# Performance work log

Hardware: AMD Instinct MI355X
Metric: run time of the kernel (lower is better)

## Reference

```python
import jax, jax.numpy as jnp
import numpy as np

N, D, T = 8192, 512, 12
EPS = 1e-6


def _ln(x, g, b):
    m = jnp.mean(x, axis=-1, keepdims=True)
    v = jnp.mean((x - m) ** 2, axis=-1, keepdims=True)
    return (x - m) / jnp.sqrt(v + EPS) * g + b


def _cross(x1, x2, Wa, ba, Wb, bb, d1, d2):
    # attn_weights2: [N, N], softmax over dim=1 (rows)
    aw2 = jax.nn.softmax((x1 @ Wa.T + ba) @ x2.T, axis=1)
    fused_x2 = (aw2 @ x2) / jnp.sqrt(jnp.float32(d2))
    aw1 = jax.nn.softmax((x2 @ Wb.T + bb) @ x1.T, axis=1)
    fused_x1 = (aw1 @ x1) / jnp.sqrt(jnp.float32(d1))
    return fused_x1, fused_x2


def setup_inputs() -> dict:
    key = jax.random.key(0)
    ks = jax.random.split(key, 16)
    s = 1.0 / np.sqrt(D)
    inp = {
        'xp': jax.random.normal(ks[0], (N, D), jnp.float32),
        'xm': jax.random.normal(ks[1], (N, D), jnp.float32),
        'xs': jax.random.normal(ks[2], (N, D), jnp.float32),
        'ln_g': jnp.ones((D,), jnp.float32),
        'ln_b': jnp.zeros((D,), jnp.float32),
        # mol cross-attention: linear1 (D->D), linear2 (D->D)
        'W1': jax.random.uniform(ks[3], (D, D), jnp.float32, -s, s),
        'b1': jnp.zeros((D,), jnp.float32),
        'W2': jax.random.uniform(ks[4], (D, D), jnp.float32, -s, s),
        'b2': jnp.zeros((D,), jnp.float32),
        # smile cross-attention
        'W3': jax.random.uniform(ks[5], (D, D), jnp.float32, -s, s),
        'b3': jnp.zeros((D,), jnp.float32),
        'W4': jax.random.uniform(ks[6], (D, D), jnp.float32, -s, s),
        'b4': jnp.zeros((D,), jnp.float32),
        # pred head: 2D -> T
        'Wp': jax.random.uniform(ks[7], (T, 2 * D), jnp.float32, -1.0 / np.sqrt(2 * D), 1.0 / np.sqrt(2 * D)),
        'bp': jnp.zeros((T,), jnp.float32),
        # gate
        't': jnp.full((1,), 0.5, jnp.float32),
        'Wt1': jax.random.uniform(ks[8], (50, 1), jnp.float32, -1.0, 1.0),
        'bt1': jnp.zeros((50,), jnp.float32),
        'Wt2': jax.random.uniform(ks[9], (1, 50), jnp.float32, -1.0 / np.sqrt(50), 1.0 / np.sqrt(50)),
        'bt2': jnp.zeros((1,), jnp.float32),
    }
    return inp


def reference(xp, xm, xs, ln_g, ln_b, W1, b1, W2, b2, W3, b3, W4, b4, Wp, bp, t, Wt1, bt1, Wt2, bt2):
    x1 = _ln(xp, ln_g, ln_b)
    x2 = _ln(xm, ln_g, ln_b)
    x3 = x1  # protein encoded twice with same LayerNorm
    x4 = _ln(xs, ln_g, ln_b)

    f1, f2 = _cross(x1, x2, W1, b1, W2, b2, D, D)
    h12 = jnp.concatenate([f1 + x1, f2 + x2], axis=1)          # [N, 2D]
    out12 = jax.nn.relu(h12) @ Wp.T + bp                        # [N, T]

    f3, f4 = _cross(x3, x4, W3, b3, W4, b4, D, D)
    h34 = jnp.concatenate([f3 + x3, f4 + x4], axis=1)
    out34 = jax.nn.relu(h34) @ Wp.T + bp

    t1 = t @ Wt1.T + bt1                                        # [50]
    t2 = jax.nn.sigmoid(t1 @ Wt2.T + bt2)                       # [1]
    return t2 * out12 + (1.0 - t2) * out34
```

## Files before the change

### kernel.cpp

```cpp
#include <hip/hip_runtime.h>
#include <stdint.h>


#define DEV __device__ __forceinline__
typedef unsigned short u16;
typedef __bf16 bf16x8 __attribute__((ext_vector_type(8)));
typedef float f32x4 __attribute__((ext_vector_type(4)));

constexpr int NR = 8192;
constexpr int DDIM = 512;
constexpr int TOUT = 12;

DEV u16 f2b(float f) {
  uint32_t u = __builtin_bit_cast(uint32_t, f);
  u += 0x7fffu + ((u >> 16) & 1u);
  return (u16)(u >> 16);
}
DEV float b2f(u16 h) {
  uint32_t u = ((uint32_t)h) << 16;
  return __builtin_bit_cast(float, u);
}

__global__ __launch_bounds__(64) void ln_kernel(
    const float* __restrict__ xp, const float* __restrict__ xm,
    const float* __restrict__ xs, const float* __restrict__ g,
    const float* __restrict__ b, u16* __restrict__ o1, u16* __restrict__ o2,
    u16* __restrict__ o4) {
  int row = blockIdx.x;
  int which = blockIdx.y;
  const float* x = which == 0 ? xp : (which == 1 ? xm : xs);
  u16* o = which == 0 ? o1 : (which == 1 ? o2 : o4);
  int lane = threadIdx.x;
  const float4* xr = (const float4*)(x + (size_t)row * DDIM);
  float4 v0 = xr[lane * 2], v1 = xr[lane * 2 + 1];
  float vals[8] = {v0.x, v0.y, v0.z, v0.w, v1.x, v1.y, v1.z, v1.w};
  float s = 0.f, s2 = 0.f;
  for (int j = 0; j < 8; j++) { s += vals[j]; s2 += vals[j] * vals[j]; }
  for (int off = 1; off < 64; off <<= 1) {
    s += __shfl_xor(s, off);
    s2 += __shfl_xor(s2, off);
  }
  float m = s * (1.0f / DDIM);
  float var = s2 * (1.0f / DDIM) - m * m;
  var = fmaxf(var, 0.f);
  float rs = rsqrtf(var + 1e-6f);
  int d0 = lane * 8;
  u16 us[8];
  for (int j = 0; j < 8; j++)
    us[j] = f2b((vals[j] - m) * rs * g[d0 + j] + b[d0 + j]);
  uint4 pk;
  pk.x = (uint32_t)us[0] | ((uint32_t)us[1] << 16);
  pk.y = (uint32_t)us[2] | ((uint32_t)us[3] << 16);
  pk.z = (uint32_t)us[4] | ((uint32_t)us[5] << 16);
  pk.w = (uint32_t)us[6] | ((uint32_t)us[7] << 16);
  *(uint4*)(o + (size_t)row * DDIM + d0) = pk;
}

__global__ __launch_bounds__(256) void wconv_kernel(
    const float* __restrict__ W1, const float* __restrict__ W2,
    const float* __restrict__ W3, const float* __restrict__ W4,
    u16* __restrict__ Wb) {
  int wi = blockIdx.y;
  const float* W = wi == 0 ? W1 : (wi == 1 ? W2 : (wi == 2 ? W3 : W4));
  size_t base = ((size_t)blockIdx.x * 256 + threadIdx.x) * 8;
  const float4* src = (const float4*)(W + base);
  float4 a = src[0], c = src[1];
  float vals[8] = {a.x, a.y, a.z, a.w, c.x, c.y, c.z, c.w};
  u16 us[8];
  for (int j = 0; j < 8; j++) us[j] = f2b(vals[j]);
  uint4 pk;
  pk.x = (uint32_t)us[0] | ((uint32_t)us[1] << 16);
  pk.y = (uint32_t)us[2] | ((uint32_t)us[3] << 16);
  pk.z = (uint32_t)us[4] | ((uint32_t)us[5] << 16);
  pk.w = (uint32_t)us[6] | ((uint32_t)us[7] << 16);
  *(uint4*)(Wb + (size_t)wi * DDIM * DDIM + base) = pk;
}

__global__ __launch_bounds__(256) void transpose_kernel(
    const u16* __restrict__ s1, const u16* __restrict__ s2,
    const u16* __restrict__ s4, u16* __restrict__ t1, u16* __restrict__ t2,
    u16* __restrict__ t4) {
  constexpr int LD = 66;
  __shared__ u16 tile[64 * LD];
  int which = blockIdx.z;
  const u16* src = which == 0 ? s1 : (which == 1 ? s2 : s4);
  u16* dst = which == 0 ? t1 : (which == 1 ? t2 : t4);
  int c0 = blockIdx.x * 64;
  int r0 = blockIdx.y * 64;
  int tid = threadIdx.x;
  for (int c = tid; c < 512; c += 256) {
    int i = c >> 3, j8 = (c & 7) * 8;
    uint4 v = *(const uint4*)(src + (size_t)(r0 + i) * DDIM + c0 + j8);
    uint32_t* dw = (uint32_t*)&tile[i * LD + j8];
    dw[0] = v.x; dw[1] = v.y; dw[2] = v.z; dw[3] = v.w;
  }
  __syncthreads();
  for (int c = tid; c < 512; c += 256) {
    int o = c >> 3, e8 = (c & 7) * 8;
    u16 us[8];
    for (int k = 0; k < 8; k++) us[k] = tile[(e8 + k) * LD + o];
    uint4 pk;
    pk.x = (uint32_t)us[0] | ((uint32_t)us[1] << 16);
    pk.y = (uint32_t)us[2] | ((uint32_t)us[3] << 16);
    pk.z = (uint32_t)us[4] | ((uint32_t)us[5] << 16);
    pk.w = (uint32_t)us[6] | ((uint32_t)us[7] << 16);
    *(uint4*)(dst + (size_t)(c0 + o) * NR + r0 + e8) = pk;
  }
}

template <int MODE>
DEV void gemm_core(const u16* __restrict__ A, const u16* __restrict__ B,
                   u16* __restrict__ C, const float* __restrict__ bias,
                   u16* lds, int K, int lda, int ldb, int ldc, int bx,
                   int by) {
  constexpr int TM = 4, TN = 4;
  u16* Asm = lds;
  u16* Bsm = lds + 4096;
  int tid = threadIdx.x;
  int w = tid >> 6, lane = tid & 63;
  int q = lane >> 4, c16 = lane & 15;
  int n0 = bx * 128, m0 = by * 128;
  int wrow = (w >> 1) * 64, wcol = (w & 1) * 64;
  f32x4 acc[TM][TN] = {};
  for (int k0 = 0; k0 < K; k0 += 32) {
    __syncthreads();
    for (int call = w; call < 16; call += 4) {
      bool isA = call < 8;
      int ci = isA ? call : call - 8;
      int chunk = ci * 64 + lane;
      int row = chunk >> 2;
      int gch = ((chunk & 3) - (row >> 1)) & 3;
      const u16* gp = isA ? (A + (size_t)(m0 + row) * lda + k0 + gch * 8)
                          : (B + (size_t)(n0 + row) * ldb + k0 + gch * 8);
      u16* lp = (isA ? Asm : Bsm) + ci * 512;
      __builtin_amdgcn_global_load_lds(
          (const __attribute__((address_space(1))) void*)gp,
          (__attribute__((address_space(3))) void*)lp, 16, 0, 0);
    }
    __syncthreads();
    bf16x8 af[TM], bfr[TN];
    for (int i = 0; i < TM; i++) {
      int r = wrow + i * 16 + c16;
      af[i] = *(const bf16x8*)&Asm[r * 32 + (((q + (r >> 1)) & 3) * 8)];
    }
    for (int n = 0; n < TN; n++) {
      int r = wcol + n * 16 + c16;
      bfr[n] = *(const bf16x8*)&Bsm[r * 32 + (((q + (r >> 1)) & 3) * 8)];
    }
    for (int i = 0; i < TM; i++)
      for (int n = 0; n < TN; n++)
        acc[i][n] = __builtin_amdgcn_mfma_f32_16x16x32_bf16(af[i], bfr[n],
                                                            acc[i][n], 0, 0, 0);
  }
  for (int h = 0; h < 2; h++) {
    __syncthreads();
    if ((w & 1) == h) {
      for (int i = 0; i < TM; i++) {
        for (int n = 0; n < TN; n++) {
          float bv = 0.f;
          if constexpr (MODE == 0) bv = bias[n0 + wcol + n * 16 + c16];
          for (int r = 0; r < 4; r++) {
            int rl = wrow + i * 16 + q * 4 + r;
            int cl = (n * 16 + c16) ^ ((rl & 7) << 3);
            float v = acc[i][n][r];
            if constexpr (MODE == 0) v += bv;
            if constexpr (MODE == 1) v = __expf(v - 48.0f);
            lds[rl * 64 + cl] = f2b(v);
          }
        }
      }
    }
    __syncthreads();
    for (int rep = 0; rep < 4; rep++) {
      int idx = rep * 256 + tid;
      int row = idx >> 3, seg = idx & 7;
      uint4 vv = ((const uint4*)lds)[row * 8 + (seg ^ (row & 7))];
      *(uint4*)(C + (size_t)(m0 + row) * ldc + n0 + h * 64 + seg * 8) = vv;
    }
  }
}

DEV void pv_body(const u16* __restrict__ A, const u16* __restrict__ B,
                 u16* lds, u16* __restrict__ C, int bx, int by) {
  constexpr int BM = 64, BN = 128, BK = 64;
  int tid = threadIdx.x, w = tid >> 6, lane = tid & 63;
  int q = lane >> 4, c16 = lane & 15;
  int n0 = bx * BN, m0 = by * BM;
  int wr = (w >> 1) * 32, wc = (w & 1) * 64;
  f32x4 acc[2][4] = {};
  f32x4 accl[2] = {};
  bf16x8 ones;
  for (int j = 0; j < 8; j++) ones[j] = (__bf16)1.0f;

  auto stage = [&](int k0, int buf) {
    for (int it = 0; it < 6; it++) {
      int cb = it * 256 + w * 64;
      int c = cb + lane;
      bool isA = cb < 512;
      int ci = isA ? c : c - 512;
      int row = ci >> 3;
      int koff = ((ci & 7) ^ (row & 7)) * 8;
      const u16* gp = isA ? (A + (size_t)(m0 + row) * NR + k0 + koff)
                          : (B + (size_t)(n0 + row) * NR + k0 + koff);
      u16* lp = isA ? (lds + buf * 4096 + cb * 8)
                    : (lds + 8192 + buf * 8192 + (cb - 512) * 8);
      __builtin_amdgcn_global_load_lds(
          (const __attribute__((address_space(1))) void*)gp,
          (__attribute__((address_space(3))) void*)lp, 16, 0, 0);
    }
  };

  stage(0, 0);
  __syncthreads();
  constexpr int KSTEPS = NR / BK;
  for (int ks = 0; ks < KSTEPS; ks++) {
    int cur = ks & 1;
    if (ks + 1 < KSTEPS) stage((ks + 1) * BK, cur ^ 1);
    const u16* Asm = lds + cur * 4096;
    const u16* Bsm = lds + 8192 + cur * 8192;
    for (int kh = 0; kh < 2; kh++) {
      bf16x8 af[2], bfr[4];
      int cl = kh * 4 + q;
      for (int i = 0; i < 2; i++) {
        int r = wr + i * 16 + c16;
        af[i] = *(const bf16x8*)&Asm[r * BK + ((cl ^ (r & 7)) * 8)];
      }
      for (int n = 0; n < 4; n++) {
        int r = wc + n * 16 + c16;
        bfr[n] = *(const bf16x8*)&Bsm[r * BK + ((cl ^ (r & 7)) * 8)];
      }
      for (int i = 0; i < 2; i++)
        accl[i] = __builtin_amdgcn_mfma_f32_16x16x32_bf16(af[i], ones, accl[i],
                                                          0, 0, 0);
      for (int i = 0; i < 2; i++)
        for (int n = 0; n < 4; n++)
          acc[i][n] = __builtin_amdgcn_mfma_f32_16x16x32_bf16(
              af[i], bfr[n], acc[i][n], 0, 0, 0);
    }
    __syncthreads();
  }
  for (int i = 0; i < 2; i++) {
    float invl[4];
    for (int r = 0; r < 4; r++)
      invl[r] = 0.044194173824159216f / accl[i][r];
    for (int n = 0; n < 4; n++) {
      int col = n0 + wc + n * 16 + c16;
      for (int r = 0; r < 4; r++) {
        int row = m0 + wr + i * 16 + q * 4 + r;
        C[(size_t)row * DDIM + col] = f2b(acc[i][n][r] * invl[r]);
      }
    }
  }
}

__global__ __launch_bounds__(256, 4) void scores_kernel(
    const u16* __restrict__ Q, const u16* __restrict__ Kv,
    u16* __restrict__ P) {
  __shared__ u16 lds[8192];
  gemm_core<1>(Q, Kv, P, nullptr, lds, DDIM, DDIM, DDIM, NR, blockIdx.x,
               blockIdx.y);
}

__global__ __launch_bounds__(256, 4) void qproj_kernel(
    const u16* __restrict__ s0, const u16* __restrict__ s1,
    const u16* __restrict__ s2, const u16* __restrict__ s3,
    const u16* __restrict__ Wb, const float* __restrict__ b0,
    const float* __restrict__ b1, const float* __restrict__ b2,
    const float* __restrict__ b3, u16* __restrict__ Qs) {
  __shared__ u16 lds[8192];
  int z = blockIdx.z;
  const u16* A = z == 0 ? s0 : (z == 1 ? s1 : (z == 2 ? s2 : s3));
  const float* bias = z == 0 ? b0 : (z == 1 ? b1 : (z == 2 ? b2 : b3));
  gemm_core<0>(A, Wb + (size_t)z * DDIM * DDIM, Qs + (size_t)z * NR * DDIM,
               bias, lds, DDIM, DDIM, DDIM, DDIM, blockIdx.x, blockIdx.y);
}

__global__ __launch_bounds__(256, 3) void pv_kernel(
    const u16* __restrict__ A, const u16* __restrict__ B,
    u16* __restrict__ C) {
  __shared__ u16 lds[24576];
  pv_body(A, B, lds, C, blockIdx.x, blockIdx.y);
}

__global__ __launch_bounds__(256, 3) void combo_kernel(
    const u16* __restrict__ Pin, const u16* __restrict__ Vt,
    u16* __restrict__ F, const u16* __restrict__ Q,
    const u16* __restrict__ Kv, u16* __restrict__ Pout) {
  __shared__ u16 lds[24576];
  if (blockIdx.x < 512) {
    pv_body(Pin, Vt, lds, F, blockIdx.x & 3, blockIdx.x >> 2);
  } else {
    int b = blockIdx.x - 512;
    gemm_core<1>(Q, Kv, Pout, nullptr, lds, DDIM, DDIM, DDIM, NR, b & 63,
                 b >> 6);
  }
}

__global__ __launch_bounds__(256) void head_kernel(
    const u16* __restrict__ F1, const u16* __restrict__ F2,
    const u16* __restrict__ F3, const u16* __restrict__ F4,
    const u16* __restrict__ x1, const u16* __restrict__ x2,
    const u16* __restrict__ x4, const float* __restrict__ Wp,
    const float* __restrict__ bp, const float* __restrict__ tg,
    const float* __restrict__ Wt1, const float* __restrict__ bt1,
    const float* __restrict__ Wt2, const float* __restrict__ bt2,
    float* __restrict__ out) {
  __shared__ float wps[TOUT * 2 * DDIM];
  __shared__ float t2s;
  int tid = threadIdx.x;
  for (int i = tid; i < TOUT * 2 * DDIM; i += 256) wps[i] = Wp[i];
  if (tid == 0) {
    float s = bt2[0];
    for (int k = 0; k < 50; k++) s += Wt2[k] * (tg[0] * Wt1[k] + bt1[k]);
    t2s = 1.0f / (1.0f + __expf(-s));
  }
  __syncthreads();
  int g = tid >> 5, j = tid & 31;
  size_t m = (size_t)blockIdx.x * 8 + g;
  float a12[TOUT] = {}, a34[TOUT] = {};
  for (int d = j; d < 2 * DDIM; d += 32) {
    float h12, h34;
    if (d < DDIM) {
      float xv = b2f(x1[m * DDIM + d]);
      h12 = b2f(F1[m * DDIM + d]) + xv;
      h34 = b2f(F3[m * DDIM + d]) + xv;
    } else {
      int dd = d - DDIM;
      h12 = b2f(F2[m * DDIM + dd]) + b2f(x2[m * DDIM + dd]);
      h34 = b2f(F4[m * DDIM + dd]) + b2f(x4[m * DDIM + dd]);
    }
    h12 = fmaxf(h12, 0.f);
    h34 = fmaxf(h34, 0.f);
    for (int t = 0; t < TOUT; t++) {
      float wv = wps[t * 2 * DDIM + d];
      a12[t] += h12 * wv;
      a34[t] += h34 * wv;
    }
  }
  for (int off = 1; off < 32; off <<= 1)
    for (int t = 0; t < TOUT; t++) {
      a12[t] += __shfl_xor(a12[t], off);
      a34[t] += __shfl_xor(a34[t], off);
    }
  if (j < TOUT) {
    float t2 = t2s;
    out[m * TOUT + j] = t2 * a12[j] + (1.f - t2) * a34[j] + bp[j];
  }
}

extern "C" void kernel_launch(void* const* d_in, const int* in_sizes, int n_in,
                              void* d_out, int out_size, void* d_ws,
                              size_t ws_size, hipStream_t stream) {
  (void)in_sizes; (void)n_in; (void)out_size;
  const float* xp = (const float*)d_in[0];
  const float* xm = (const float*)d_in[1];
  const float* xs = (const float*)d_in[2];
  const float* ln_g = (const float*)d_in[3];
  const float* ln_b = (const float*)d_in[4];
  const float* Wmat[4] = {(const float*)d_in[5], (const float*)d_in[7],
                          (const float*)d_in[9], (const float*)d_in[11]};
  const float* bvec[4] = {(const float*)d_in[6], (const float*)d_in[8],
                          (const float*)d_in[10], (const float*)d_in[12]};
  const float* Wp = (const float*)d_in[13];
  const float* bp = (const float*)d_in[14];
  const float* tg = (const float*)d_in[15];
  const float* Wt1 = (const float*)d_in[16];
  const float* bt1 = (const float*)d_in[17];
  const float* Wt2 = (const float*)d_in[18];
  const float* bt2 = (const float*)d_in[19];
  float* out = (float*)d_out;

  char* ws = (char*)d_ws;
  const size_t MB = 1ull << 20;
  u16* x1b = (u16*)(ws + 0 * MB);
  u16* x2b = (u16*)(ws + 8 * MB);
  u16* x4b = (u16*)(ws + 16 * MB);
  u16* x1t = (u16*)(ws + 24 * MB);
  u16* x2t = (u16*)(ws + 32 * MB);
  u16* x4t = (u16*)(ws + 40 * MB);
  u16* Wb = (u16*)(ws + 48 * MB);
  u16* Qs = (u16*)(ws + 52 * MB);
  u16* P0 = (u16*)(ws + 84 * MB);
  bool dual = ws_size >= 340 * MB;
  u16* P1 = dual ? (u16*)(ws + 212 * MB) : P0;

  ln_kernel<<<dim3(NR, 3), 64, 0, stream>>>(xp, xm, xs, ln_g, ln_b, x1b, x2b,
                                            x4b);
  wconv_kernel<<<dim3(128, 4), 256, 0, stream>>>(Wmat[0], Wmat[1], Wmat[2],
                                                 Wmat[3], Wb);
  transpose_kernel<<<dim3(8, 128, 3), 256, 0, stream>>>(x1b, x2b, x4b, x1t,
                                                        x2t, x4t);
  qproj_kernel<<<dim3(DDIM / 128, NR / 128, 4), 256, 0, stream>>>(
      x1b, x2b, x1b, x4b, Wb, bvec[0], bvec[1], bvec[2], bvec[3], Qs);

  const u16* kvb[4] = {x2b, x1b, x4b, x1b};
  const u16* kvt[4] = {x2t, x1t, x4t, x1t};
  u16* slot[4];
  for (int a = 0; a < 4; a++) slot[a] = Qs + (size_t)a * NR * DDIM;

  if (dual) {
    u16* Pb[4] = {P0, P1, P0, P1};
    scores_kernel<<<dim3(64, 64), 256, 0, stream>>>(slot[0], kvb[0], Pb[0]);
    for (int a = 0; a < 3; a++) {
      combo_kernel<<<dim3(512 + 64 * 64), 256, 0, stream>>>(
          Pb[a], kvt[a], slot[a], slot[a + 1], kvb[a + 1], Pb[a + 1]);
    }
    pv_kernel<<<dim3(4, 128), 256, 0, stream>>>(Pb[3], kvt[3], slot[3]);
  } else {
    for (int a = 0; a < 4; a++) {
      scores_kernel<<<dim3(64, 64), 256, 0, stream>>>(slot[a], kvb[a], P0);
      pv_kernel<<<dim3(4, 128), 256, 0, stream>>>(P0, kvt[a], slot[a]);
    }
  }

  head_kernel<<<dim3(NR / 8), 256, 0, stream>>>(
      slot[1], slot[0], slot[3], slot[2], x1b, x2b, x4b, Wp, bp, tg, Wt1, bt1,
      Wt2, bt2, out);
}
```

Before: 1.036 ms.

## Triple-stage PV loads with explicit waitcnt and fuse remaining Q projections with first scores

The PV loop now prefetches two k-steps ahead, using explicit vmcnt waits and raw barriers in place of __syncthreads, so global-to-LDS loads overlap more with MFMA work. The qproj launch is cut to the first projection only. The other three projections run in a new combined kernel with the first scores GEMM, which replaces the separate scores launch and fills the GPU with more blocks. The transpose loop change is cosmetic. The hand-written waitcnt counts are fragile if the number of loads per stage changes.

```diff
diff --git a/kernel.cpp b/kernel.cpp
--- a/kernel.cpp
+++ b/kernel.cpp
@@ -95,16 +95,17 @@
     dw[0] = v.x; dw[1] = v.y; dw[2] = v.z; dw[3] = v.w;
   }
   __syncthreads();
-  for (int c = tid; c < 512; c += 256) {
-    int o = c >> 3, e8 = (c & 7) * 8;
+  for (int rep = 0; rep < 2; rep++) {
+    int idx = rep * 256 + tid;
+    int o = idx >> 3, j8 = (idx & 7) * 8;
     u16 us[8];
-    for (int k = 0; k < 8; k++) us[k] = tile[(e8 + k) * LD + o];
+    for (int k = 0; k < 8; k++) us[k] = tile[(j8 + k) * LD + o];
     uint4 pk;
     pk.x = (uint32_t)us[0] | ((uint32_t)us[1] << 16);
     pk.y = (uint32_t)us[2] | ((uint32_t)us[3] << 16);
     pk.z = (uint32_t)us[4] | ((uint32_t)us[5] << 16);
     pk.w = (uint32_t)us[6] | ((uint32_t)us[7] << 16);
-    *(uint4*)(dst + (size_t)(c0 + o) * NR + r0 + e8) = pk;
+    *(uint4*)(dst + (size_t)(c0 + o) * NR + r0 + j8) = pk;
   }
 }
 
@@ -210,12 +211,18 @@
     }
   };
 
+  constexpr int KSTEPS = NR / BK;
   stage(0, 0);
-  __syncthreads();
-  constexpr int KSTEPS = NR / BK;
+  stage(BK, 1);
   for (int ks = 0; ks < KSTEPS; ks++) {
     int cur = ks & 1;
-    if (ks + 1 < KSTEPS) stage((ks + 1) * BK, cur ^ 1);
+    if (ks + 1 < KSTEPS)
+      asm volatile("s_waitcnt vmcnt(6)" ::: "memory");
+    else
+      asm volatile("s_waitcnt vmcnt(0)" ::: "memory");
+    __builtin_amdgcn_sched_barrier(0);
+    __builtin_amdgcn_s_barrier();
+    __builtin_amdgcn_sched_barrier(0);
     const u16* Asm = lds + cur * 4096;
     const u16* Bsm = lds + 8192 + cur * 8192;
     for (int kh = 0; kh < 2; kh++) {
@@ -237,7 +244,11 @@
           acc[i][n] = __builtin_amdgcn_mfma_f32_16x16x32_bf16(
               af[i], bfr[n], acc[i][n], 0, 0, 0);
     }
-    __syncthreads();
+    asm volatile("s_waitcnt lgkmcnt(0)" ::: "memory");
+    __builtin_amdgcn_sched_barrier(0);
+    __builtin_amdgcn_s_barrier();
+    __builtin_amdgcn_sched_barrier(0);
+    if (ks + 2 < KSTEPS) stage((ks + 2) * BK, cur);
   }
   for (int i = 0; i < 2; i++) {
     float invl[4];
@@ -273,6 +284,27 @@
   const float* bias = z == 0 ? b0 : (z == 1 ? b1 : (z == 2 ? b2 : b3));
   gemm_core<0>(A, Wb + (size_t)z * DDIM * DDIM, Qs + (size_t)z * NR * DDIM,
                bias, lds, DDIM, DDIM, DDIM, DDIM, blockIdx.x, blockIdx.y);
+}
+
+__global__ __launch_bounds__(256, 4) void qscombo_kernel(
+    const u16* __restrict__ x1b, const u16* __restrict__ x2b,
+    const u16* __restrict__ x4b, const u16* __restrict__ Wb,
+    const float* __restrict__ b1, const float* __restrict__ b2,
+    const float* __restrict__ b3, u16* __restrict__ Qs,
+    const u16* __restrict__ Q0, u16* __restrict__ P) {
+  __shared__ u16 lds[8192];
+  if (blockIdx.x < 768) {
+    int b = blockIdx.x;
+    int z = 1 + (b >> 8), rem = b & 255;
+    const u16* A = z == 1 ? x2b : (z == 2 ? x1b : x4b);
+    const float* bias = z == 1 ? b1 : (z == 2 ? b2 : b3);
+    gemm_core<0>(A, Wb + (size_t)z * DDIM * DDIM, Qs + (size_t)z * NR * DDIM,
+                 bias, lds, DDIM, DDIM, DDIM, DDIM, rem & 3, rem >> 2);
+  } else {
+    int b = blockIdx.x - 768;
+    gemm_core<1>(Q0, x2b, P, nullptr, lds, DDIM, DDIM, DDIM, NR, b & 63,
+                 b >> 6);
+  }
 }
 
 __global__ __launch_bounds__(256, 3) void pv_kernel(
@@ -390,7 +422,7 @@
                                                  Wmat[3], Wb);
   transpose_kernel<<<dim3(8, 128, 3), 256, 0, stream>>>(x1b, x2b, x4b, x1t,
                                                         x2t, x4t);
-  qproj_kernel<<<dim3(DDIM / 128, NR / 128, 4), 256, 0, stream>>>(
+  qproj_kernel<<<dim3(DDIM / 128, NR / 128, 1), 256, 0, stream>>>(
       x1b, x2b, x1b, x4b, Wb, bvec[0], bvec[1], bvec[2], bvec[3], Qs);
 
   const u16* kvb[4] = {x2b, x1b, x4b, x1b};
@@ -398,9 +430,11 @@
   u16* slot[4];
   for (int a = 0; a < 4; a++) slot[a] = Qs + (size_t)a * NR * DDIM;
 
+  qscombo_kernel<<<dim3(768 + 64 * 64), 256, 0, stream>>>(
+      x1b, x2b, x4b, Wb, bvec[1], bvec[2], bvec[3], Qs, slot[0], P0);
+
   if (dual) {
     u16* Pb[4] = {P0, P1, P0, P1};
-    scores_kernel<<<dim3(64, 64), 256, 0, stream>>>(slot[0], kvb[0], Pb[0]);
     for (int a = 0; a < 3; a++) {
       combo_kernel<<<dim3(512 + 64 * 64), 256, 0, stream>>>(
           Pb[a], kvt[a], slot[a], slot[a + 1], kvb[a + 1], Pb[a + 1]);
@@ -408,7 +442,8 @@
     pv_kernel<<<dim3(4, 128), 256, 0, stream>>>(Pb[3], kvt[3], slot[3]);
   } else {
     for (int a = 0; a < 4; a++) {
-      scores_kernel<<<dim3(64, 64), 256, 0, stream>>>(slot[a], kvb[a], P0);
+      if (a > 0)
+        scores_kernel<<<dim3(64, 64), 256, 0, stream>>>(slot[a], kvb[a], P0);
       pv_kernel<<<dim3(4, 128), 256, 0, stream>>>(P0, kvt[a], slot[a]);
     }
   }
```

Result: faster. 995.7 us (-3.8%).
